# Optimization experiments

Hardware: AMD Instinct MI355X
Metric: run time of the kernel (lower is better)

The kernel has to match this reference:

```python
import jax, jax.numpy as jnp
import numpy as np

H = 64           # edge/node/global hidden size
IN_F = 4         # node_attr_size
OUT_F = 1        # out_size
NUM_EMB = 100    # edge_num_embeddings
SKIP = True


def setup_inputs() -> dict:
    key = jax.random.key(0)
    ks = jax.random.split(key, 24)
    T, N, E = 4, 20000, 320000
    NNZ = 340000
    inp = {
        'node_attr': jax.random.normal(ks[0], (T, N, IN_F), jnp.float32),
        'global_attr': jax.random.normal(ks[1], (1, H), jnp.float32),
        'L_values': jax.random.normal(ks[2], (NNZ,), jnp.float32),
        'coeff': jnp.ones((1,), jnp.float32),
        'edge_attr': jax.random.randint(ks[3], (T, E), 0, NUM_EMB),
        'edge_index': jax.random.randint(ks[4], (2, E), 0, N),
        'L_index': jax.random.randint(ks[5], (2, NNZ), 0, N),
        'num_processing_steps': 4,
        # parameters
        'emb': jax.random.normal(ks[6], (NUM_EMB, H), jnp.float32) * 0.05,
        'W_ne': jax.random.normal(ks[7], (IN_F, H), jnp.float32) * 0.1,
        'b_ne': jnp.zeros((H,), jnp.float32),
        'W_eb': jax.random.normal(ks[8], ((H + 2 * H) * 2 + H, H), jnp.float32) * 0.05,
        'b_eb': jnp.zeros((H,), jnp.float32),
        'W_nb': jax.random.normal(ks[9], (2 * H + 2 * H + H, H), jnp.float32) * 0.05,
        'b_nb': jnp.zeros((H,), jnp.float32),
        'W_gb': jax.random.normal(ks[10], (H + H + H, H), jnp.float32) * 0.05,
        'b_gb': jnp.zeros((H,), jnp.float32),
        'W_d1': jax.random.normal(ks[11], (H, H), jnp.float32) * 0.1,
        'b_d1': jnp.zeros((H,), jnp.float32),
        'W_d2': jax.random.normal(ks[12], (H, OUT_F), jnp.float32) * 0.1,
        'b_d2': jnp.zeros((OUT_F,), jnp.float32),
        'W_i1': jax.random.normal(ks[13], (H, H), jnp.float32) * 0.1,
        'b_i1': jnp.zeros((H,), jnp.float32),
        'W_i2': jax.random.normal(ks[14], (H, IN_F), jnp.float32) * 0.1,
        'b_i2': jnp.zeros((IN_F,), jnp.float32),
    }
    return inp


def reference(node_attr, global_attr, L_values, coeff, emb, W_ne, b_ne,
              W_eb, b_eb, W_nb, b_nb, W_gb, b_gb, W_d1, b_d1, W_d2, b_d2,
              W_i1, b_i1, W_i2, b_i2, edge_attr, edge_index, L_index,
              num_processing_steps):
    T, N, _ = node_attr.shape
    s, r = edge_index[0], edge_index[1]
    Li, Lj = L_index[0], L_index[1]

    # encoders (all T steps at once)
    x_enc = jax.nn.relu(node_attr @ W_ne + b_ne)   # [T,N,H]
    e_enc = emb[edge_attr]                         # [T,E,H]

    def laplacian(h):  # sparse sp_L @ h, h: [N,H]
        return jax.ops.segment_sum(L_values[:, None] * h[Lj], Li, num_segments=N)

    def step(carry, xe):
        h_x, h_e, h_g = carry
        x_t, e_t = xe
        node_cat = jnp.concatenate([x_t, h_x], axis=-1)          # [N,2H]
        edge_cat = jnp.concatenate([e_t, h_e], axis=-1)          # [E,2H]
        g = h_g[0]                                               # [H]
        E_ = edge_cat.shape[0]
        # EdgeBlock: edges + sender + receiver + globals
        eb_in = jnp.concatenate([edge_cat, node_cat[s], node_cat[r],
                                 jnp.broadcast_to(g, (E_, g.shape[0]))], axis=-1)
        e_new = jax.nn.relu(eb_in @ W_eb + b_eb)                 # [E,H]
        # NodeBlock: scatter_add aggregates of received/sent edges
        recv = jax.ops.segment_sum(e_new, r, num_segments=N)
        sent = jax.ops.segment_sum(e_new, s, num_segments=N)
        nb_in = jnp.concatenate([recv, sent, node_cat,
                                 jnp.broadcast_to(g, (N, g.shape[0]))], axis=-1)
        x_new = jax.nn.relu(nb_in @ W_nb + b_nb)                 # [N,H]
        # GlobalBlock: scatter_mean (single graph -> mean)
        gb_in = jnp.concatenate([e_new.mean(0), x_new.mean(0), g])[None]
        g_new = jax.nn.relu(gb_in @ W_gb + b_gb)                 # [1,H]
        h_x_next = h_x + x_new if SKIP else x_new
        time_d = h_x_next - h_x
        spat_d = coeff[0] * laplacian(h_x_next)  # pde='diff': coeff * L u
        return (h_x_next, e_new, g_new), (h_x_next, time_d, spat_d)

    h0 = (jnp.zeros((N, H), jnp.float32),
          jnp.zeros((e_enc.shape[1], H), jnp.float32),
          global_attr)
    _, (hid, time_d, spat_d) = jax.lax.scan(step, h0, (x_enc, e_enc))

    # decoders over all steps
    out_nodes = jax.nn.relu(hid @ W_d1 + b_d1) @ W_d2 + b_d2     # [T,N,OUT_F]
    pred_in = jax.nn.relu(hid @ W_i1 + b_i1) @ W_i2 + b_i2       # [T,N,IN_F]
    return out_nodes, time_d, spat_d, pred_in
```

## Files before the change

kernel.cpp:

```cpp
#include <hip/hip_runtime.h>

#define TT 4
#define NN 20000
#define EE 320000
#define NZ 340000
#define NBKT 2500

typedef __attribute__((ext_vector_type(8))) __bf16 bf16x8;
typedef __attribute__((ext_vector_type(16))) float f32x16;

__device__ __forceinline__ unsigned short f2bf(float f) {
    unsigned int u = __float_as_uint(f);
    u = (u + 0x7FFFu + ((u >> 16) & 1u)) >> 16;
    return (unsigned short)u;
}
__device__ __forceinline__ float bf2f(unsigned short h) {
    return __uint_as_float(((unsigned int)h) << 16);
}

#define GLL16(src, dst) __builtin_amdgcn_global_load_lds( \
    (const __attribute__((address_space(1))) unsigned int*)(src), \
    (__attribute__((address_space(3))) unsigned int*)(dst), 16, 0, 0)

__global__ void k_count(const int* __restrict__ r, const int* __restrict__ s,
                        const int* __restrict__ Li,
                        int* cnt_r, int* cnt_s, int* cnt_L) {
    int i = blockIdx.x * 256 + threadIdx.x;
    if (i < EE) { atomicAdd(&cnt_r[r[i]], 1); atomicAdd(&cnt_s[s[i]], 1); }
    if (i < NZ) { atomicAdd(&cnt_L[Li[i]], 1); }
}

__global__ __launch_bounds__(1024) void k_scan(int* cnt, int* rowp, int* wp) {
    int which = blockIdx.x;
    int* c = cnt + which * NN;
    int* row = rowp + which * (NN + 1);
    int* w = wp + which * NN;
    __shared__ int ssum[1024];
    int tid = threadIdx.x;
    const int CH = (NN + 1023) / 1024;
    int base = tid * CH;
    int s = 0;
    for (int i = 0; i < CH; ++i) { int idx = base + i; s += (idx < NN) ? c[idx] : 0; }
    ssum[tid] = s;
    __syncthreads();
    for (int o = 1; o < 1024; o <<= 1) {
        int v = (tid >= o) ? ssum[tid - o] : 0;
        __syncthreads();
        ssum[tid] += v;
        __syncthreads();
    }
    int run = (tid > 0) ? ssum[tid - 1] : 0;
    for (int i = 0; i < CH; ++i) {
        int idx = base + i;
        if (idx < NN) { row[idx] = run; w[idx] = run; run += c[idx]; }
    }
    if (tid == 1023) row[NN] = ssum[1023];
}

__global__ __launch_bounds__(256) void k_scatter(
    const int* __restrict__ r, const int* __restrict__ s,
    const int* __restrict__ Li, const int* __restrict__ Lj,
    const float* __restrict__ Lv,
    int* wp_r, int* wp_s, int* wp_L,
    int* col_r, int* col_s, uint2* col_L8) {
    const int bucket = blockIdx.x & 7;
    const int nlo = bucket * NBKT;
    const int cid = blockIdx.x >> 3;
    const int stride = (gridDim.x >> 3) * 256;
    for (int i = cid * 256 + threadIdx.x; i < EE; i += stride) {
        int rv = r[i];
        if ((unsigned)(rv - nlo) < (unsigned)NBKT)
            col_r[atomicAdd(&wp_r[rv], 1)] = i;
        int sv = s[i];
        if ((unsigned)(sv - nlo) < (unsigned)NBKT)
            col_s[atomicAdd(&wp_s[sv], 1)] = i;
    }
    for (int i = cid * 256 + threadIdx.x; i < NZ; i += stride) {
        int lv = Li[i];
        if ((unsigned)(lv - nlo) < (unsigned)NBKT) {
            int pos = atomicAdd(&wp_L[lv], 1);
            uint2 v;
            v.x = (unsigned int)Lj[i];
            v.y = __float_as_uint(Lv[i]);
            col_L8[pos] = v;
        }
    }
}

__global__ __launch_bounds__(256) void k_pack(
    const float* __restrict__ W_eb, const float* __restrict__ W_nb,
    const float* __restrict__ W_d1, const float* __restrict__ W_i1,
    const float* __restrict__ emb, unsigned short* __restrict__ Bpe,
    unsigned short* __restrict__ Bpu, unsigned short* __restrict__ Bpn,
    unsigned short* __restrict__ Bpd, unsigned short* __restrict__ emb_bf) {
    int t = blockIdx.x * 256 + threadIdx.x;
    if (t < 2 * 8 * 512) {
        int i = t & 7, l = (t >> 3) & 63, kb = (t >> 9) & 7, ch = t >> 12;
        int colv = ch * 32 + (l & 31);
        int k = kb * 16 + (l >> 5) * 8 + i;
        Bpe[t] = f2bf(W_eb[k * 64 + colv]);
    }
    if (t < 4 * 8 * 512) {
        int i = t & 7, l = (t >> 3) & 63, kb = (t >> 9) & 7, g = t >> 12;
        int colv = (g & 1) * 32 + (l & 31);
        int k = 128 + (g >> 1) * 128 + kb * 16 + (l >> 5) * 8 + i;
        Bpu[t] = f2bf(W_eb[k * 64 + colv]);
    }
    if (t < 2 * 16 * 512) {
        int i = t & 7, l = (t >> 3) & 63, kb = (t >> 9) % 16, ch = t / (16 * 512);
        int colv = ch * 32 + (l & 31);
        int k = kb * 16 + (l >> 5) * 8 + i;
        Bpn[t] = f2bf(W_nb[k * 64 + colv]);
    }
    if (t < 4 * 4 * 512) {
        int i = t & 7, l = (t >> 3) & 63, kb = (t >> 9) & 3, sec = t >> 11;
        int colv = (sec & 1) * 32 + (l & 31);
        int k = kb * 16 + (l >> 5) * 8 + i;
        const float* W = (sec < 2) ? W_d1 : W_i1;
        Bpd[t] = f2bf(W[k * 64 + colv]);
    }
    if (t < 100 * 64) emb_bf[t] = f2bf(emb[t]);
}

__global__ __launch_bounds__(256) void k_xenc(const float* __restrict__ na,
                                              const float* __restrict__ W_ne,
                                              const float* __restrict__ b_ne,
                                              unsigned short* __restrict__ xenc) {
    int row = blockIdx.x * 4 + (threadIdx.x >> 6);
    int j = threadIdx.x & 63;
    float4 a = *(const float4*)&na[(size_t)row * 4];
    float v = b_ne[j] + a.x * W_ne[j] + a.y * W_ne[64 + j] + a.z * W_ne[128 + j] + a.w * W_ne[192 + j];
    xenc[(size_t)row * 64 + j] = f2bf(fmaxf(v, 0.f));
}

__global__ __launch_bounds__(64) void k_usr(
    int do_update,
    const unsigned short* __restrict__ xenc_t, const unsigned short* __restrict__ hx_bf,
    const unsigned short* __restrict__ Bpu, unsigned int* __restrict__ usr,
    const float* __restrict__ W_gb, const float* __restrict__ b_gb,
    const float* __restrict__ W_eb, const float* __restrict__ b_eb,
    const float* __restrict__ W_nb, const float* __restrict__ b_nb,
    float* __restrict__ g_cur, float* __restrict__ e_sum, float* __restrict__ x_sum,
    float* __restrict__ gb_eb, float* __restrict__ gb_nb) {
    const int ln = threadIdx.x;
    const int er = ln & 31, hi = ln >> 5;

    if (blockIdx.x == 0) {
        int j = ln;
        float gv = g_cur[j];
        if (do_update) {
            float a = b_gb[j];
            for (int k = 0; k < 64; ++k) a += (e_sum[k] / (float)EE) * W_gb[k * 64 + j];
            for (int k = 0; k < 64; ++k) a += (x_sum[k] / (float)NN) * W_gb[(64 + k) * 64 + j];
            for (int k = 0; k < 64; ++k) a += g_cur[k] * W_gb[(128 + k) * 64 + j];
            gv = fmaxf(a, 0.f);
            g_cur[j] = gv;
            e_sum[j] = 0.f;
            x_sum[j] = 0.f;
        }
        float a1 = b_eb[j], a2 = b_nb[j];
        for (int k = 0; k < 64; ++k) {
            float gk = __shfl(gv, k, 64);
            a1 = fmaf(gk, W_eb[(384 + k) * 64 + j], a1);
            a2 = fmaf(gk, W_nb[(256 + k) * 64 + j], a2);
        }
        gb_eb[j] = a1;
        gb_nb[j] = a2;
    }

    const int n0 = blockIdx.x * 32;
    const int n = n0 + er;

    f32x16 a0, a1, a2, a3;
    #pragma unroll
    for (int i = 0; i < 16; ++i) { a0[i] = 0.f; a1[i] = 0.f; a2[i] = 0.f; a3[i] = 0.f; }

    const unsigned short* sx = xenc_t + (size_t)64 * n + hi * 8;
    const unsigned short* sh = hx_bf + (size_t)64 * n + hi * 8;
    #pragma unroll
    for (int c = 0; c < 2; ++c) {
        const unsigned short* src = c ? sh : sx;
        #pragma unroll
        for (int kb = 0; kb < 4; ++kb) {
            bf16x8 a = *(const bf16x8*)(src + kb * 16);
            int kg = c * 4 + kb;
            bf16x8 b0 = *(const bf16x8*)&Bpu[(size_t)((0 * 8 + kg) * 64 + ln) * 8];
            bf16x8 b1 = *(const bf16x8*)&Bpu[(size_t)((1 * 8 + kg) * 64 + ln) * 8];
            bf16x8 b2 = *(const bf16x8*)&Bpu[(size_t)((2 * 8 + kg) * 64 + ln) * 8];
            bf16x8 b3 = *(const bf16x8*)&Bpu[(size_t)((3 * 8 + kg) * 64 + ln) * 8];
            a0 = __builtin_amdgcn_mfma_f32_32x32x16_bf16(a, b0, a0, 0, 0, 0);
            a1 = __builtin_amdgcn_mfma_f32_32x32x16_bf16(a, b1, a1, 0, 0, 0);
            a2 = __builtin_amdgcn_mfma_f32_32x32x16_bf16(a, b2, a2, 0, 0, 0);
            a3 = __builtin_amdgcn_mfma_f32_32x32x16_bf16(a, b3, a3, 0, 0, 0);
        }
    }
    #pragma unroll
    for (int r = 0; r < 16; ++r) {
        int row = (r & 3) + 8 * (r >> 2) + 4 * hi;
        size_t o = (size_t)(n0 + row) * 64;
        usr[o + er]      = (unsigned int)f2bf(a0[r]) | ((unsigned int)f2bf(a1[r]) << 16);
        usr[o + 32 + er] = (unsigned int)f2bf(a2[r]) | ((unsigned int)f2bf(a3[r]) << 16);
    }
}

__global__ __launch_bounds__(512) void k_edge(
    int first, unsigned short* __restrict__ h_e,
    const unsigned short* __restrict__ emb_bf,
    const unsigned int* __restrict__ usr, const int* __restrict__ eattr_t,
    const int* __restrict__ sidx, const int* __restrict__ ridx,
    const unsigned short* __restrict__ Bp, const float* __restrict__ gbias,
    float* __restrict__ e_sum) {
    __shared__ unsigned short sBe[8192];
    __shared__ float sRed[8][64];
    const int tid = threadIdx.x;
    const int w = tid >> 6, ln = tid & 63;
    const int er = ln & 31, hi = ln >> 5;
    const int ebase = blockIdx.x * 256 + w * 32;
    const int e = ebase + er;

    const int siv = sidx[ebase + er];
    const int riv = ridx[ebase + er];
    const int ai = eattr_t[e];

    #pragma unroll
    for (int i = 0; i < 2; ++i) {
        int off = i * 4096 + w * 512;
        GLL16(Bp + off + ln * 8, sBe + off);
    }

    const unsigned short* s0 = emb_bf + (size_t)64 * ai + hi * 8;
    const unsigned short* s1 = h_e + (size_t)64 * e + hi * 8;
    bf16x8 a0 = *(const bf16x8*)(s0);
    bf16x8 a1 = *(const bf16x8*)(s0 + 16);
    bf16x8 a2 = *(const bf16x8*)(s0 + 32);
    bf16x8 a3 = *(const bf16x8*)(s0 + 48);
    bf16x8 a4{}, a5{}, a6{}, a7{};
    if (!first) {
        a4 = *(const bf16x8*)(s1);
        a5 = *(const bf16x8*)(s1 + 16);
        a6 = *(const bf16x8*)(s1 + 32);
        a7 = *(const bf16x8*)(s1 + 48);
    }

    f32x16 acc0, acc1;
    #pragma unroll
    for (int i = 0; i < 16; ++i) { acc0[i] = 0.f; acc1[i] = 0.f; }

    __syncthreads();

    #define EMM(AF, KG)                                                              \
        {                                                                            \
            bf16x8 b0 = *(const bf16x8*)&sBe[(((KG)) * 64 + ln) * 8];                \
            bf16x8 b1 = *(const bf16x8*)&sBe[((8 + (KG)) * 64 + ln) * 8];            \
            acc0 = __builtin_amdgcn_mfma_f32_32x32x16_bf16(AF, b0, acc0, 0, 0, 0);   \
            acc1 = __builtin_amdgcn_mfma_f32_32x32x16_bf16(AF, b1, acc1, 0, 0, 0);   \
        }
    EMM(a0, 0) EMM(a1, 1) EMM(a2, 2) EMM(a3, 3)
    if (!first) {
        EMM(a4, 4) EMM(a5, 5) EMM(a6, 6) EMM(a7, 7)
    }
    #undef EMM

    const float gb0 = gbias[er], gb1 = gbias[er + 32];
    float cs0 = 0.f, cs1 = 0.f;
    #pragma unroll
    for (int r = 0; r < 16; ++r) {
        int row = (r & 3) + 8 * (r >> 2) + 4 * hi;
        int si_row = __shfl(siv, row, 64);
        int ri_row = __shfl(riv, row, 64);
        unsigned int us = usr[(size_t)si_row * 64 + er];
        unsigned int ur = usr[(size_t)ri_row * 64 + 32 + er];
        size_t o = (size_t)(ebase + row) * 64;
        float v0 = fmaxf(acc0[r] + bf2f((unsigned short)(us & 0xFFFF))
                                 + bf2f((unsigned short)(ur & 0xFFFF)) + gb0, 0.f);
        float v1 = fmaxf(acc1[r] + bf2f((unsigned short)(us >> 16))
                                 + bf2f((unsigned short)(ur >> 16)) + gb1, 0.f);
        cs0 += v0; cs1 += v1;
        h_e[o + er] = f2bf(v0);
        h_e[o + er + 32] = f2bf(v1);
    }
    cs0 += __shfl_xor(cs0, 32, 64);
    cs1 += __shfl_xor(cs1, 32, 64);
    if (hi == 0) { sRed[w][er] = cs0; sRed[w][er + 32] = cs1; }
    __syncthreads();
    if (w == 0) {
        float t = 0.f;
        #pragma unroll
        for (int q = 0; q < 8; ++q) t += sRed[q][ln];
        atomicAdd(&e_sum[ln], t);
    }
}

__global__ __launch_bounds__(256) void k_gather(
    const unsigned short* __restrict__ h_e, const int* __restrict__ row_r,
    const int* __restrict__ col_r, const int* __restrict__ row_s,
    const int* __restrict__ col_s, unsigned short* __restrict__ recv,
    unsigned short* __restrict__ sentb) {
    int t = blockIdx.x * 256 + threadIdx.x;
    int sub = t & 31, n = t >> 5;
    int g = sub & 15, which = sub >> 4;
    const int* rowp = which ? row_s : row_r;
    const int* colp = which ? col_s : col_r;
    unsigned short* outp = which ? sentb : recv;

    float a0 = 0.f, a1 = 0.f, a2 = 0.f, a3 = 0.f;
    int b0 = rowp[n], b1 = rowp[n + 1];
    for (int p = b0; p < b1; ++p) {
        uint2 v = *(const uint2*)&h_e[(size_t)64 * colp[p] + g * 4];
        a0 += bf2f((unsigned short)(v.x & 0xFFFF));
        a1 += bf2f((unsigned short)(v.x >> 16));
        a2 += bf2f((unsigned short)(v.y & 0xFFFF));
        a3 += bf2f((unsigned short)(v.y >> 16));
    }
    uint2 packed;
    packed.x = (unsigned int)f2bf(a0) | ((unsigned int)f2bf(a1) << 16);
    packed.y = (unsigned int)f2bf(a2) | ((unsigned int)f2bf(a3) << 16);
    *(uint2*)&outp[(size_t)64 * n + g * 4] = packed;
}

#define NODE_CHUNK(CIDX, BASE)                                                          \
    {                                                                                   \
        const unsigned short* src = (BASE) + hi * 8;                                    \
        _Pragma("unroll") for (int kb = 0; kb < 4; ++kb) {                              \
            bf16x8 a = *(const bf16x8*)(src + kb * 16);                                 \
            bf16x8 b0 = *(const bf16x8*)&Bp[(size_t)(((CIDX)*4 + kb) * 64 + ln) * 8];   \
            bf16x8 b1 = *(const bf16x8*)&Bp[(size_t)((16 + (CIDX)*4 + kb) * 64 + ln) * 8]; \
            acc0 = __builtin_amdgcn_mfma_f32_32x32x16_bf16(a, b0, acc0, 0, 0, 0);       \
            acc1 = __builtin_amdgcn_mfma_f32_32x32x16_bf16(a, b1, acc1, 0, 0, 0);       \
        }                                                                               \
    }

__global__ __launch_bounds__(64) void k_node(
    const unsigned short* __restrict__ recv, const unsigned short* __restrict__ sentb,
    const unsigned short* __restrict__ xenc_t, float* __restrict__ h_x,
    unsigned short* __restrict__ hx_bf, const unsigned short* __restrict__ Bp,
    const float* __restrict__ gbias, float* __restrict__ x_sum,
    unsigned short* __restrict__ hid_t, float* __restrict__ timed_t) {
    const int ln = threadIdx.x;
    const int er = ln & 31, hi = ln >> 5;
    const int n0 = blockIdx.x * 32;
    const int n = n0 + er;

    f32x16 acc0, acc1;
    #pragma unroll
    for (int i = 0; i < 16; ++i) { acc0[i] = 0.f; acc1[i] = 0.f; }

    NODE_CHUNK(0, recv + (size_t)64 * n)
    NODE_CHUNK(1, sentb + (size_t)64 * n)
    NODE_CHUNK(2, xenc_t + (size_t)64 * n)
    NODE_CHUNK(3, hx_bf + (size_t)64 * n)

    const float gb0 = gbias[er], gb1 = gbias[er + 32];
    float cs0 = 0.f, cs1 = 0.f;
    #pragma unroll
    for (int r = 0; r < 16; ++r) {
        int row = (r & 3) + 8 * (r >> 2) + 4 * hi;
        size_t o = (size_t)(n0 + row) * 64;
        float x0 = fmaxf(acc0[r] + gb0, 0.f);
        float x1 = fmaxf(acc1[r] + gb1, 0.f);
        cs0 += x0; cs1 += x1;
        float hx0 = h_x[o + er] + x0;
        float hx1 = h_x[o + er + 32] + x1;
        unsigned short hb0 = f2bf(hx0), hb1 = f2bf(hx1);
        h_x[o + er] = hx0;        h_x[o + er + 32] = hx1;
        hx_bf[o + er] = hb0;      hx_bf[o + er + 32] = hb1;
        hid_t[o + er] = hb0;      hid_t[o + er + 32] = hb1;
        timed_t[o + er] = x0;     timed_t[o + er + 32] = x1;
    }
    cs0 += __shfl_xor(cs0, 32, 64);
    cs1 += __shfl_xor(cs1, 32, 64);
    if (hi == 0) {
        atomicAdd(&x_sum[er], cs0);
        atomicAdd(&x_sum[er + 32], cs1);
    }
}

__global__ __launch_bounds__(256) void k_lap(
    const unsigned short* __restrict__ hx_bf, const int* __restrict__ row_L,
    const uint2* __restrict__ col_L8, const float* __restrict__ coeff,
    float* __restrict__ spat_t) {
    int t = blockIdx.x * 256 + threadIdx.x;
    int sub = t & 31, n = t >> 5;
    int g = sub & 15, half = sub >> 4;
    float a0 = 0.f, a1 = 0.f, a2 = 0.f, a3 = 0.f;
    int b0 = row_L[n], b1 = row_L[n + 1];
    int mid = b0 + ((b1 - b0) >> 1);
    int p0 = half ? mid : b0;
    int p1 = half ? b1 : mid;
    for (int p = p0; p < p1; ++p) {
        uint2 e = col_L8[p];
        float lv = __uint_as_float(e.y);
        uint2 hv = *(const uint2*)&hx_bf[(size_t)64 * e.x + g * 4];
        a0 = fmaf(lv, bf2f((unsigned short)(hv.x & 0xFFFF)), a0);
        a1 = fmaf(lv, bf2f((unsigned short)(hv.x >> 16)), a1);
        a2 = fmaf(lv, bf2f((unsigned short)(hv.y & 0xFFFF)), a2);
        a3 = fmaf(lv, bf2f((unsigned short)(hv.y >> 16)), a3);
    }
    a0 += __shfl_xor(a0, 16, 64);
    a1 += __shfl_xor(a1, 16, 64);
    a2 += __shfl_xor(a2, 16, 64);
    a3 += __shfl_xor(a3, 16, 64);
    if (half == 0) {
        float c = coeff[0];
        float4 outv = {c * a0, c * a1, c * a2, c * a3};
        *(float4*)&spat_t[(size_t)64 * n + g * 4] = outv;
    }
}

__global__ __launch_bounds__(256) void k_dec(
    const unsigned short* __restrict__ hid_bf, const unsigned short* __restrict__ Bpd,
    const float* __restrict__ b_d1, const float* __restrict__ W_d2,
    const float* __restrict__ b_d2, const float* __restrict__ b_i1,
    const float* __restrict__ W_i2, const float* __restrict__ b_i2,
    float* __restrict__ out_nodes, float* __restrict__ pred_in) {
    __shared__ unsigned short sDec[4][32 * 138];
    const int tid = threadIdx.x;
    const int w = tid >> 6, ln = tid & 63;
    const int er = ln & 31, hi = ln >> 5;
    const int row0 = (blockIdx.x * 4 + w) * 32;

    f32x16 ad0, ad1, ai0, ai1;
    #pragma unroll
    for (int i = 0; i < 16; ++i) { ad0[i] = 0.f; ad1[i] = 0.f; ai0[i] = 0.f; ai1[i] = 0.f; }

    const unsigned short* src = hid_bf + (size_t)(row0 + er) * 64 + hi * 8;
    #pragma unroll
    for (int kb = 0; kb < 4; ++kb) {
        bf16x8 a = *(const bf16x8*)(src + kb * 16);
        bf16x8 bd0 = *(const bf16x8*)&Bpd[((0 * 4 + kb) * 64 + ln) * 8];
        bf16x8 bd1 = *(const bf16x8*)&Bpd[((4 + kb) * 64 + ln) * 8];
        bf16x8 bi0 = *(const bf16x8*)&Bpd[((8 + kb) * 64 + ln) * 8];
        bf16x8 bi1 = *(const bf16x8*)&Bpd[((12 + kb) * 64 + ln) * 8];
        ad0 = __builtin_amdgcn_mfma_f32_32x32x16_bf16(a, bd0, ad0, 0, 0, 0);
        ad1 = __builtin_amdgcn_mfma_f32_32x32x16_bf16(a, bd1, ad1, 0, 0, 0);
        ai0 = __builtin_amdgcn_mfma_f32_32x32x16_bf16(a, bi0, ai0, 0, 0, 0);
        ai1 = __builtin_amdgcn_mfma_f32_32x32x16_bf16(a, bi1, ai1, 0, 0, 0);
    }

    const float bd0v = b_d1[er], bd1v = b_d1[er + 32];
    const float bi0v = b_i1[er], bi1v = b_i1[er + 32];
    unsigned short* sw = &sDec[w][0];
    #pragma unroll
    for (int r = 0; r < 16; ++r) {
        int row = (r & 3) + 8 * (r >> 2) + 4 * hi;
        sw[row * 138 + er]       = f2bf(fmaxf(ad0[r] + bd0v, 0.f));
        sw[row * 138 + er + 32]  = f2bf(fmaxf(ad1[r] + bd1v, 0.f));
        sw[row * 138 + er + 64]  = f2bf(fmaxf(ai0[r] + bi0v, 0.f));
        sw[row * 138 + er + 96]  = f2bf(fmaxf(ai1[r] + bi1v, 0.f));
    }
    __syncthreads();

    const int g_row = row0 + er;
    if (hi == 0) {
        float s = 0.f;
        for (int k = 0; k < 32; ++k) {
            unsigned int u = *(const unsigned int*)&sw[er * 138 + 2 * k];
            s = fmaf(bf2f((unsigned short)(u & 0xFFFF)), W_d2[2 * k], s);
            s = fmaf(bf2f((unsigned short)(u >> 16)), W_d2[2 * k + 1], s);
        }
        out_nodes[g_row] = s + b_d2[0];
    } else {
        float s0 = 0.f, s1 = 0.f, s2 = 0.f, s3 = 0.f;
        for (int k = 0; k < 32; ++k) {
            unsigned int u = *(const unsigned int*)&sw[er * 138 + 64 + 2 * k];
            float vlo = bf2f((unsigned short)(u & 0xFFFF));
            float vhi = bf2f((unsigned short)(u >> 16));
            float4 w0 = *(const float4*)&W_i2[(2 * k) * 4];
            float4 w1 = *(const float4*)&W_i2[(2 * k + 1) * 4];
            s0 = fmaf(vlo, w0.x, fmaf(vhi, w1.x, s0));
            s1 = fmaf(vlo, w0.y, fmaf(vhi, w1.y, s1));
            s2 = fmaf(vlo, w0.z, fmaf(vhi, w1.z, s2));
            s3 = fmaf(vlo, w0.w, fmaf(vhi, w1.w, s3));
        }
        float4 pv = {s0 + b_i2[0], s1 + b_i2[1], s2 + b_i2[2], s3 + b_i2[3]};
        *(float4*)&pred_in[(size_t)4 * g_row] = pv;
    }
}

extern "C" void kernel_launch(void* const* d_in, const int* in_sizes, int n_in,
                              void* d_out, int out_size, void* d_ws, size_t ws_size,
                              hipStream_t stream) {
    (void)in_sizes; (void)n_in; (void)out_size; (void)ws_size;
    const float* node_attr   = (const float*)d_in[0];
    const float* global_attr = (const float*)d_in[1];
    const float* L_values    = (const float*)d_in[2];
    const float* coeff       = (const float*)d_in[3];
    const int*   edge_attr   = (const int*)d_in[4];
    const int*   edge_index  = (const int*)d_in[5];
    const int*   L_index     = (const int*)d_in[6];
    const float* emb  = (const float*)d_in[8];
    const float* W_ne = (const float*)d_in[9];
    const float* b_ne = (const float*)d_in[10];
    const float* W_eb = (const float*)d_in[11];
    const float* b_eb = (const float*)d_in[12];
    const float* W_nb = (const float*)d_in[13];
    const float* b_nb = (const float*)d_in[14];
    const float* W_gb = (const float*)d_in[15];
    const float* b_gb = (const float*)d_in[16];
    const float* W_d1 = (const float*)d_in[17];
    const float* b_d1 = (const float*)d_in[18];
    const float* W_d2 = (const float*)d_in[19];
    const float* b_d2 = (const float*)d_in[20];
    const float* W_i1 = (const float*)d_in[21];
    const float* b_i1 = (const float*)d_in[22];
    const float* W_i2 = (const float*)d_in[23];
    const float* b_i2 = (const float*)d_in[24];

    const int* s_idx = edge_index;
    const int* r_idx = edge_index + EE;
    const int* Li = L_index;
    const int* Lj = L_index + NZ;

    char* ws = (char*)d_ws;
    size_t off = 0;
    auto alloc = [&](size_t bytes) -> void* {
        void* p = ws + off;
        off = (off + bytes + 255) & ~(size_t)255;
        return p;
    };
    unsigned short* xenc   = (unsigned short*)alloc((size_t)TT * NN * 64 * 2);
    unsigned short* hid    = (unsigned short*)alloc((size_t)TT * NN * 64 * 2);
    float*          h_x    = (float*)alloc((size_t)NN * 64 * 4);
    unsigned short* hx_bf  = (unsigned short*)alloc((size_t)NN * 64 * 2);
    unsigned short* h_e    = (unsigned short*)alloc((size_t)EE * 64 * 2);
    unsigned short* recv   = (unsigned short*)alloc((size_t)NN * 64 * 2);
    unsigned short* sentb  = (unsigned short*)alloc((size_t)NN * 64 * 2);
    unsigned int*   usr    = (unsigned int*)alloc((size_t)NN * 64 * 4);
    float* smalls          = (float*)alloc(2048);
    unsigned short* Bpe    = (unsigned short*)alloc((size_t)2 * 8 * 512 * 2);
    unsigned short* Bpu    = (unsigned short*)alloc((size_t)4 * 8 * 512 * 2);
    unsigned short* Bpn    = (unsigned short*)alloc((size_t)2 * 16 * 512 * 2);
    unsigned short* Bpd    = (unsigned short*)alloc((size_t)4 * 4 * 512 * 2);
    unsigned short* emb_bf = (unsigned short*)alloc((size_t)100 * 64 * 2);
    int* cnt    = (int*)alloc((size_t)3 * NN * 4);
    int* rowp   = (int*)alloc((size_t)3 * (NN + 1) * 4);
    int* wp     = (int*)alloc((size_t)3 * NN * 4);
    int* col_r  = (int*)alloc((size_t)EE * 4);
    int* col_s  = (int*)alloc((size_t)EE * 4);
    uint2* col_L8 = (uint2*)alloc((size_t)NZ * 8);

    float* g_cur = smalls;
    float* e_sum = smalls + 64;
    float* x_sum = smalls + 128;
    float* gb_eb = smalls + 192;
    float* gb_nb = smalls + 256;
    int* cnt_r = cnt, *cnt_s = cnt + NN, *cnt_L = cnt + 2 * NN;
    int* row_r = rowp, *row_s = rowp + (NN + 1), *row_L = rowp + 2 * (NN + 1);
    int* wp_r = wp, *wp_s = wp + NN, *wp_L = wp + 2 * NN;

    float* out_nodes = (float*)d_out;
    float* time_d = out_nodes + (size_t)TT * NN;
    float* spat_d = time_d + (size_t)TT * NN * 64;
    float* pred_in = spat_d + (size_t)TT * NN * 64;

    hipMemsetAsync(h_x, 0, (size_t)NN * 64 * 4, stream);
    hipMemsetAsync(hx_bf, 0, (size_t)NN * 64 * 2, stream);
    hipMemsetAsync(smalls, 0, 2048, stream);
    hipMemsetAsync(cnt, 0, (size_t)3 * NN * 4, stream);
    hipMemcpyAsync(g_cur, global_attr, 64 * 4, hipMemcpyDeviceToDevice, stream);

    k_count<<<(NZ + 255) / 256, 256, 0, stream>>>(r_idx, s_idx, Li, cnt_r, cnt_s, cnt_L);
    k_scan<<<3, 1024, 0, stream>>>(cnt, rowp, wp);
    k_scatter<<<2048, 256, 0, stream>>>(r_idx, s_idx, Li, Lj, L_values,
                                        wp_r, wp_s, wp_L, col_r, col_s, col_L8);
    k_pack<<<96, 256, 0, stream>>>(W_eb, W_nb, W_d1, W_i1, emb,
                                   Bpe, Bpu, Bpn, Bpd, emb_bf);
    k_xenc<<<TT * NN / 4, 256, 0, stream>>>(node_attr, W_ne, b_ne, xenc);

    for (int t = 0; t < TT; ++t) {
        const unsigned short* xenc_t = xenc + (size_t)t * NN * 64;
        k_usr<<<NN / 32, 64, 0, stream>>>(t > 0, xenc_t, hx_bf, Bpu, usr,
                                          W_gb, b_gb, W_eb, b_eb, W_nb, b_nb,
                                          g_cur, e_sum, x_sum, gb_eb, gb_nb);
        k_edge<<<EE / 256, 512, 0, stream>>>(t == 0, h_e, emb_bf, usr,
                                             edge_attr + (size_t)t * EE, s_idx, r_idx,
                                             Bpe, gb_eb, e_sum);
        k_gather<<<NN * 32 / 256, 256, 0, stream>>>(h_e, row_r, col_r, row_s, col_s,
                                                    recv, sentb);
        k_node<<<NN / 32, 64, 0, stream>>>(recv, sentb, xenc_t, h_x, hx_bf,
                                           Bpn, gb_nb, x_sum,
                                           hid + (size_t)t * NN * 64,
                                           time_d + (size_t)t * NN * 64);
        k_lap<<<NN * 32 / 256, 256, 0, stream>>>(hx_bf, row_L, col_L8, coeff,
                                                 spat_d + (size_t)t * NN * 64);
    }
    k_dec<<<TT * NN / 128, 256, 0, stream>>>(hid, Bpd, b_d1, W_d2, b_d2,
                                             b_i1, W_i2, b_i2, out_nodes, pred_in);
}
```

Baseline: 675.9 us.

## Fuse Laplacian SpMV with next-step node-update GEMM into one launch

The per-step Laplacian kernel and the following step's usr GEMM/global-update kernel become one launch that splits blocks by role: the first LAPB blocks do the SpMV and the rest do the usr work for step t+1. The usr path moves from 64-thread blocks to 256-thread blocks with four waves each. The CSR-build kernels also switch index loads to nontemporal loads. This removes launches and lets the two independent pieces of work overlap on the GPU. The global update still runs in the last step's fused launch because it resets e_sum and x_sum.

```diff
diff --git a/kernel.cpp b/kernel.cpp
--- a/kernel.cpp
+++ b/kernel.cpp
@@ -5,6 +5,7 @@
 #define EE 320000
 #define NZ 340000
 #define NBKT 2500
+#define LAPB 2500
 
 typedef __attribute__((ext_vector_type(8))) __bf16 bf16x8;
 typedef __attribute__((ext_vector_type(16))) float f32x16;
@@ -26,8 +27,11 @@
                         const int* __restrict__ Li,
                         int* cnt_r, int* cnt_s, int* cnt_L) {
     int i = blockIdx.x * 256 + threadIdx.x;
-    if (i < EE) { atomicAdd(&cnt_r[r[i]], 1); atomicAdd(&cnt_s[s[i]], 1); }
-    if (i < NZ) { atomicAdd(&cnt_L[Li[i]], 1); }
+    if (i < EE) {
+        atomicAdd(&cnt_r[__builtin_nontemporal_load(&r[i])], 1);
+        atomicAdd(&cnt_s[__builtin_nontemporal_load(&s[i])], 1);
+    }
+    if (i < NZ) { atomicAdd(&cnt_L[__builtin_nontemporal_load(&Li[i])], 1); }
 }
 
 __global__ __launch_bounds__(1024) void k_scan(int* cnt, int* rowp, int* wp) {
@@ -68,20 +72,20 @@
     const int cid = blockIdx.x >> 3;
     const int stride = (gridDim.x >> 3) * 256;
     for (int i = cid * 256 + threadIdx.x; i < EE; i += stride) {
-        int rv = r[i];
+        int rv = __builtin_nontemporal_load(&r[i]);
         if ((unsigned)(rv - nlo) < (unsigned)NBKT)
             col_r[atomicAdd(&wp_r[rv], 1)] = i;
-        int sv = s[i];
+        int sv = __builtin_nontemporal_load(&s[i]);
         if ((unsigned)(sv - nlo) < (unsigned)NBKT)
             col_s[atomicAdd(&wp_s[sv], 1)] = i;
     }
     for (int i = cid * 256 + threadIdx.x; i < NZ; i += stride) {
-        int lv = Li[i];
+        int lv = __builtin_nontemporal_load(&Li[i]);
         if ((unsigned)(lv - nlo) < (unsigned)NBKT) {
             int pos = atomicAdd(&wp_L[lv], 1);
             uint2 v;
-            v.x = (unsigned int)Lj[i];
-            v.y = __float_as_uint(Lv[i]);
+            v.x = (unsigned int)__builtin_nontemporal_load(&Lj[i]);
+            v.y = __float_as_uint(__builtin_nontemporal_load(&Lv[i]));
             col_L8[pos] = v;
         }
     }
@@ -133,19 +137,54 @@
     xenc[(size_t)row * 64 + j] = f2bf(fmaxf(v, 0.f));
 }
 
-__global__ __launch_bounds__(64) void k_usr(
-    int do_update,
-    const unsigned short* __restrict__ xenc_t, const unsigned short* __restrict__ hx_bf,
-    const unsigned short* __restrict__ Bpu, unsigned int* __restrict__ usr,
+__global__ __launch_bounds__(256) void k_fuse(
+    int lapb, int nwaves_usr, int do_update,
+    const unsigned short* __restrict__ hx_bf, const int* __restrict__ row_L,
+    const uint2* __restrict__ col_L8, const float* __restrict__ coeff,
+    float* __restrict__ spat_t,
+    const unsigned short* __restrict__ xenc_next, const unsigned short* __restrict__ Bpu,
+    unsigned int* __restrict__ usr,
     const float* __restrict__ W_gb, const float* __restrict__ b_gb,
     const float* __restrict__ W_eb, const float* __restrict__ b_eb,
     const float* __restrict__ W_nb, const float* __restrict__ b_nb,
     float* __restrict__ g_cur, float* __restrict__ e_sum, float* __restrict__ x_sum,
     float* __restrict__ gb_eb, float* __restrict__ gb_nb) {
-    const int ln = threadIdx.x;
+    const int tid = threadIdx.x;
+    if ((int)blockIdx.x < lapb) {
+        int t = blockIdx.x * 256 + tid;
+        int sub = t & 31, n = t >> 5;
+        int g = sub & 15, half = sub >> 4;
+        float a0 = 0.f, a1 = 0.f, a2 = 0.f, a3 = 0.f;
+        int b0 = row_L[n], b1 = row_L[n + 1];
+        int mid = b0 + ((b1 - b0) >> 1);
+        int p0 = half ? mid : b0;
+        int p1 = half ? b1 : mid;
+        for (int p = p0; p < p1; ++p) {
+            uint2 e = col_L8[p];
+            float lv = __uint_as_float(e.y);
+            uint2 hv = *(const uint2*)&hx_bf[(size_t)64 * e.x + g * 4];
+            a0 = fmaf(lv, bf2f((unsigned short)(hv.x & 0xFFFF)), a0);
+            a1 = fmaf(lv, bf2f((unsigned short)(hv.x >> 16)), a1);
+            a2 = fmaf(lv, bf2f((unsigned short)(hv.y & 0xFFFF)), a2);
+            a3 = fmaf(lv, bf2f((unsigned short)(hv.y >> 16)), a3);
+        }
+        a0 += __shfl_xor(a0, 16, 64);
+        a1 += __shfl_xor(a1, 16, 64);
+        a2 += __shfl_xor(a2, 16, 64);
+        a3 += __shfl_xor(a3, 16, 64);
+        if (half == 0) {
+            float c = coeff[0];
+            float4 outv = {c * a0, c * a1, c * a2, c * a3};
+            *(float4*)&spat_t[(size_t)64 * n + g * 4] = outv;
+        }
+        return;
+    }
+
+    const int ln = tid & 63;
+    const int wid = ((int)blockIdx.x - lapb) * 4 + (tid >> 6);
     const int er = ln & 31, hi = ln >> 5;
 
-    if (blockIdx.x == 0) {
+    if (wid == 0) {
         int j = ln;
         float gv = g_cur[j];
         if (do_update) {
@@ -167,15 +206,16 @@
         gb_eb[j] = a1;
         gb_nb[j] = a2;
     }
-
-    const int n0 = blockIdx.x * 32;
+    if (wid >= nwaves_usr) return;
+
+    const int n0 = wid * 32;
     const int n = n0 + er;
 
     f32x16 a0, a1, a2, a3;
     #pragma unroll
     for (int i = 0; i < 16; ++i) { a0[i] = 0.f; a1[i] = 0.f; a2[i] = 0.f; a3[i] = 0.f; }
 
-    const unsigned short* sx = xenc_t + (size_t)64 * n + hi * 8;
+    const unsigned short* sx = xenc_next + (size_t)64 * n + hi * 8;
     const unsigned short* sh = hx_bf + (size_t)64 * n + hi * 8;
     #pragma unroll
     for (int c = 0; c < 2; ++c) {
@@ -372,38 +412,6 @@
     if (hi == 0) {
         atomicAdd(&x_sum[er], cs0);
         atomicAdd(&x_sum[er + 32], cs1);
-    }
-}
-
-__global__ __launch_bounds__(256) void k_lap(
-    const unsigned short* __restrict__ hx_bf, const int* __restrict__ row_L,
-    const uint2* __restrict__ col_L8, const float* __restrict__ coeff,
-    float* __restrict__ spat_t) {
-    int t = blockIdx.x * 256 + threadIdx.x;
-    int sub = t & 31, n = t >> 5;
-    int g = sub & 15, half = sub >> 4;
-    float a0 = 0.f, a1 = 0.f, a2 = 0.f, a3 = 0.f;
-    int b0 = row_L[n], b1 = row_L[n + 1];
-    int mid = b0 + ((b1 - b0) >> 1);
-    int p0 = half ? mid : b0;
-    int p1 = half ? b1 : mid;
-    for (int p = p0; p < p1; ++p) {
-        uint2 e = col_L8[p];
-        float lv = __uint_as_float(e.y);
-        uint2 hv = *(const uint2*)&hx_bf[(size_t)64 * e.x + g * 4];
-        a0 = fmaf(lv, bf2f((unsigned short)(hv.x & 0xFFFF)), a0);
-        a1 = fmaf(lv, bf2f((unsigned short)(hv.x >> 16)), a1);
-        a2 = fmaf(lv, bf2f((unsigned short)(hv.y & 0xFFFF)), a2);
-        a3 = fmaf(lv, bf2f((unsigned short)(hv.y >> 16)), a3);
-    }
-    a0 += __shfl_xor(a0, 16, 64);
-    a1 += __shfl_xor(a1, 16, 64);
-    a2 += __shfl_xor(a2, 16, 64);
-    a3 += __shfl_xor(a3, 16, 64);
-    if (half == 0) {
-        float c = coeff[0];
-        float4 outv = {c * a0, c * a1, c * a2, c * a3};
-        *(float4*)&spat_t[(size_t)64 * n + g * 4] = outv;
     }
 }
 
@@ -567,11 +575,15 @@
                                    Bpe, Bpu, Bpn, Bpd, emb_bf);
     k_xenc<<<TT * NN / 4, 256, 0, stream>>>(node_attr, W_ne, b_ne, xenc);
 
+    const int USRB = (NN / 32 + 3) / 4;
+    k_fuse<<<USRB, 256, 0, stream>>>(0, NN / 32, 0,
+                                     hx_bf, row_L, col_L8, coeff, spat_d,
+                                     xenc, Bpu, usr,
+                                     W_gb, b_gb, W_eb, b_eb, W_nb, b_nb,
+                                     g_cur, e_sum, x_sum, gb_eb, gb_nb);
+
     for (int t = 0; t < TT; ++t) {
         const unsigned short* xenc_t = xenc + (size_t)t * NN * 64;
-        k_usr<<<NN / 32, 64, 0, stream>>>(t > 0, xenc_t, hx_bf, Bpu, usr,
-                                          W_gb, b_gb, W_eb, b_eb, W_nb, b_nb,
-                                          g_cur, e_sum, x_sum, gb_eb, gb_nb);
         k_edge<<<EE / 256, 512, 0, stream>>>(t == 0, h_e, emb_bf, usr,
                                              edge_attr + (size_t)t * EE, s_idx, r_idx,
                                              Bpe, gb_eb, e_sum);
@@ -581,8 +593,16 @@
                                            Bpn, gb_nb, x_sum,
                                            hid + (size_t)t * NN * 64,
                                            time_d + (size_t)t * NN * 64);
-        k_lap<<<NN * 32 / 256, 256, 0, stream>>>(hx_bf, row_L, col_L8, coeff,
-                                                 spat_d + (size_t)t * NN * 64);
+        int nwaves = (t < TT - 1) ? NN / 32 : 0;
+        int grid = LAPB + ((t < TT - 1) ? USRB : 1);
+        const unsigned short* xenc_next =
+            xenc + (size_t)((t < TT - 1) ? t + 1 : t) * NN * 64;
+        k_fuse<<<grid, 256, 0, stream>>>(LAPB, nwaves, 1,
+                                         hx_bf, row_L, col_L8, coeff,
+                                         spat_d + (size_t)t * NN * 64,
+                                         xenc_next, Bpu, usr,
+                                         W_gb, b_gb, W_eb, b_eb, W_nb, b_nb,
+                                         g_cur, e_sum, x_sum, gb_eb, gb_nb);
     }
     k_dec<<<TT * NN / 128, 256, 0, stream>>>(hid, Bpd, b_d1, W_d2, b_d2,
                                              b_i1, W_i2, b_i2, out_nodes, pred_in);
```

Measured after the change: 716.2 us. 6.0% more time.

## Merge setup kernels and fuse the Laplacian of step t-1 into the gather of step t

Applied to the files above, without the earlier changes.

Three setup kernels (xenc encode, index counting, weight packing) become one launch that dispatches on block index. In the time loop, the Laplacian for the previous step's hidden state now runs in the same launch as the current step's edge gather. A final standalone Laplacian launch handles the last step. This cuts kernel launches and lets two independent, memory-bound gather workloads share the GPU. Correctness relies on hx_bf not being overwritten until k_node runs, which holds because k_node is launched after the fused kernel.

```diff
diff --git a/kernel.cpp b/kernel.cpp
--- a/kernel.cpp
+++ b/kernel.cpp
@@ -22,12 +22,63 @@
     (const __attribute__((address_space(1))) unsigned int*)(src), \
     (__attribute__((address_space(3))) unsigned int*)(dst), 16, 0, 0)
 
-__global__ void k_count(const int* __restrict__ r, const int* __restrict__ s,
-                        const int* __restrict__ Li,
-                        int* cnt_r, int* cnt_s, int* cnt_L) {
-    int i = blockIdx.x * 256 + threadIdx.x;
-    if (i < EE) { atomicAdd(&cnt_r[r[i]], 1); atomicAdd(&cnt_s[s[i]], 1); }
-    if (i < NZ) { atomicAdd(&cnt_L[Li[i]], 1); }
+#define XB (TT * NN / 4)
+#define CB ((NZ + 255) / 256)
+
+__global__ __launch_bounds__(256) void k_setup(
+    const float* __restrict__ na, const float* __restrict__ W_ne,
+    const float* __restrict__ b_ne, unsigned short* __restrict__ xenc,
+    const int* __restrict__ r, const int* __restrict__ s,
+    const int* __restrict__ Li, int* cnt_r, int* cnt_s, int* cnt_L,
+    const float* __restrict__ W_eb, const float* __restrict__ W_nb,
+    const float* __restrict__ W_d1, const float* __restrict__ W_i1,
+    const float* __restrict__ emb, unsigned short* __restrict__ Bpe,
+    unsigned short* __restrict__ Bpu, unsigned short* __restrict__ Bpn,
+    unsigned short* __restrict__ Bpd, unsigned short* __restrict__ emb_bf) {
+    int bid = blockIdx.x;
+    if (bid < XB) {
+        int row = bid * 4 + (threadIdx.x >> 6);
+        int j = threadIdx.x & 63;
+        float4 a = *(const float4*)&na[(size_t)row * 4];
+        float v = b_ne[j] + a.x * W_ne[j] + a.y * W_ne[64 + j] + a.z * W_ne[128 + j] + a.w * W_ne[192 + j];
+        xenc[(size_t)row * 64 + j] = f2bf(fmaxf(v, 0.f));
+        return;
+    }
+    bid -= XB;
+    if (bid < CB) {
+        int i = bid * 256 + threadIdx.x;
+        if (i < EE) { atomicAdd(&cnt_r[r[i]], 1); atomicAdd(&cnt_s[s[i]], 1); }
+        if (i < NZ) { atomicAdd(&cnt_L[Li[i]], 1); }
+        return;
+    }
+    bid -= CB;
+    int t = bid * 256 + threadIdx.x;
+    if (t < 2 * 8 * 512) {
+        int i = t & 7, l = (t >> 3) & 63, kb = (t >> 9) & 7, ch = t >> 12;
+        int colv = ch * 32 + (l & 31);
+        int k = kb * 16 + (l >> 5) * 8 + i;
+        Bpe[t] = f2bf(W_eb[k * 64 + colv]);
+    }
+    if (t < 4 * 8 * 512) {
+        int i = t & 7, l = (t >> 3) & 63, kb = (t >> 9) & 7, g = t >> 12;
+        int colv = (g & 1) * 32 + (l & 31);
+        int k = 128 + (g >> 1) * 128 + kb * 16 + (l >> 5) * 8 + i;
+        Bpu[t] = f2bf(W_eb[k * 64 + colv]);
+    }
+    if (t < 2 * 16 * 512) {
+        int i = t & 7, l = (t >> 3) & 63, kb = (t >> 9) % 16, ch = t / (16 * 512);
+        int colv = ch * 32 + (l & 31);
+        int k = kb * 16 + (l >> 5) * 8 + i;
+        Bpn[t] = f2bf(W_nb[k * 64 + colv]);
+    }
+    if (t < 4 * 4 * 512) {
+        int i = t & 7, l = (t >> 3) & 63, kb = (t >> 9) & 3, sec = t >> 11;
+        int colv = (sec & 1) * 32 + (l & 31);
+        int k = kb * 16 + (l >> 5) * 8 + i;
+        const float* W = (sec < 2) ? W_d1 : W_i1;
+        Bpd[t] = f2bf(W[k * 64 + colv]);
+    }
+    if (t < 100 * 64) emb_bf[t] = f2bf(emb[t]);
 }
 
 __global__ __launch_bounds__(1024) void k_scan(int* cnt, int* rowp, int* wp) {
@@ -87,52 +138,6 @@
     }
 }
 
-__global__ __launch_bounds__(256) void k_pack(
-    const float* __restrict__ W_eb, const float* __restrict__ W_nb,
-    const float* __restrict__ W_d1, const float* __restrict__ W_i1,
-    const float* __restrict__ emb, unsigned short* __restrict__ Bpe,
-    unsigned short* __restrict__ Bpu, unsigned short* __restrict__ Bpn,
-    unsigned short* __restrict__ Bpd, unsigned short* __restrict__ emb_bf) {
-    int t = blockIdx.x * 256 + threadIdx.x;
-    if (t < 2 * 8 * 512) {
-        int i = t & 7, l = (t >> 3) & 63, kb = (t >> 9) & 7, ch = t >> 12;
-        int colv = ch * 32 + (l & 31);
-        int k = kb * 16 + (l >> 5) * 8 + i;
-        Bpe[t] = f2bf(W_eb[k * 64 + colv]);
-    }
-    if (t < 4 * 8 * 512) {
-        int i = t & 7, l = (t >> 3) & 63, kb = (t >> 9) & 7, g = t >> 12;
-        int colv = (g & 1) * 32 + (l & 31);
-        int k = 128 + (g >> 1) * 128 + kb * 16 + (l >> 5) * 8 + i;
-        Bpu[t] = f2bf(W_eb[k * 64 + colv]);
-    }
-    if (t < 2 * 16 * 512) {
-        int i = t & 7, l = (t >> 3) & 63, kb = (t >> 9) % 16, ch = t / (16 * 512);
-        int colv = ch * 32 + (l & 31);
-        int k = kb * 16 + (l >> 5) * 8 + i;
-        Bpn[t] = f2bf(W_nb[k * 64 + colv]);
-    }
-    if (t < 4 * 4 * 512) {
-        int i = t & 7, l = (t >> 3) & 63, kb = (t >> 9) & 3, sec = t >> 11;
-        int colv = (sec & 1) * 32 + (l & 31);
-        int k = kb * 16 + (l >> 5) * 8 + i;
-        const float* W = (sec < 2) ? W_d1 : W_i1;
-        Bpd[t] = f2bf(W[k * 64 + colv]);
-    }
-    if (t < 100 * 64) emb_bf[t] = f2bf(emb[t]);
-}
-
-__global__ __launch_bounds__(256) void k_xenc(const float* __restrict__ na,
-                                              const float* __restrict__ W_ne,
-                                              const float* __restrict__ b_ne,
-                                              unsigned short* __restrict__ xenc) {
-    int row = blockIdx.x * 4 + (threadIdx.x >> 6);
-    int j = threadIdx.x & 63;
-    float4 a = *(const float4*)&na[(size_t)row * 4];
-    float v = b_ne[j] + a.x * W_ne[j] + a.y * W_ne[64 + j] + a.z * W_ne[128 + j] + a.w * W_ne[192 + j];
-    xenc[(size_t)row * 64 + j] = f2bf(fmaxf(v, 0.f));
-}
-
 __global__ __launch_bounds__(64) void k_usr(
     int do_update,
     const unsigned short* __restrict__ xenc_t, const unsigned short* __restrict__ hx_bf,
@@ -291,95 +296,39 @@
     }
 }
 
-__global__ __launch_bounds__(256) void k_gather(
+__global__ __launch_bounds__(256) void k_glap(
+    int gatherb,
     const unsigned short* __restrict__ h_e, const int* __restrict__ row_r,
     const int* __restrict__ col_r, const int* __restrict__ row_s,
     const int* __restrict__ col_s, unsigned short* __restrict__ recv,
-    unsigned short* __restrict__ sentb) {
-    int t = blockIdx.x * 256 + threadIdx.x;
-    int sub = t & 31, n = t >> 5;
-    int g = sub & 15, which = sub >> 4;
-    const int* rowp = which ? row_s : row_r;
-    const int* colp = which ? col_s : col_r;
-    unsigned short* outp = which ? sentb : recv;
-
-    float a0 = 0.f, a1 = 0.f, a2 = 0.f, a3 = 0.f;
-    int b0 = rowp[n], b1 = rowp[n + 1];
-    for (int p = b0; p < b1; ++p) {
-        uint2 v = *(const uint2*)&h_e[(size_t)64 * colp[p] + g * 4];
-        a0 += bf2f((unsigned short)(v.x & 0xFFFF));
-        a1 += bf2f((unsigned short)(v.x >> 16));
-        a2 += bf2f((unsigned short)(v.y & 0xFFFF));
-        a3 += bf2f((unsigned short)(v.y >> 16));
-    }
-    uint2 packed;
-    packed.x = (unsigned int)f2bf(a0) | ((unsigned int)f2bf(a1) << 16);
-    packed.y = (unsigned int)f2bf(a2) | ((unsigned int)f2bf(a3) << 16);
-    *(uint2*)&outp[(size_t)64 * n + g * 4] = packed;
-}
-
-#define NODE_CHUNK(CIDX, BASE)                                                          \
-    {                                                                                   \
-        const unsigned short* src = (BASE) + hi * 8;                                    \
-        _Pragma("unroll") for (int kb = 0; kb < 4; ++kb) {                              \
-            bf16x8 a = *(const bf16x8*)(src + kb * 16);                                 \
-            bf16x8 b0 = *(const bf16x8*)&Bp[(size_t)(((CIDX)*4 + kb) * 64 + ln) * 8];   \
-            bf16x8 b1 = *(const bf16x8*)&Bp[(size_t)((16 + (CIDX)*4 + kb) * 64 + ln) * 8]; \
-            acc0 = __builtin_amdgcn_mfma_f32_32x32x16_bf16(a, b0, acc0, 0, 0, 0);       \
-            acc1 = __builtin_amdgcn_mfma_f32_32x32x16_bf16(a, b1, acc1, 0, 0, 0);       \
-        }                                                                               \
-    }
-
-__global__ __launch_bounds__(64) void k_node(
-    const unsigned short* __restrict__ recv, const unsigned short* __restrict__ sentb,
-    const unsigned short* __restrict__ xenc_t, float* __restrict__ h_x,
-    unsigned short* __restrict__ hx_bf, const unsigned short* __restrict__ Bp,
-    const float* __restrict__ gbias, float* __restrict__ x_sum,
-    unsigned short* __restrict__ hid_t, float* __restrict__ timed_t) {
-    const int ln = threadIdx.x;
-    const int er = ln & 31, hi = ln >> 5;
-    const int n0 = blockIdx.x * 32;
-    const int n = n0 + er;
-
-    f32x16 acc0, acc1;
-    #pragma unroll
-    for (int i = 0; i < 16; ++i) { acc0[i] = 0.f; acc1[i] = 0.f; }
-
-    NODE_CHUNK(0, recv + (size_t)64 * n)
-    NODE_CHUNK(1, sentb + (size_t)64 * n)
-    NODE_CHUNK(2, xenc_t + (size_t)64 * n)
-    NODE_CHUNK(3, hx_bf + (size_t)64 * n)
-
-    const float gb0 = gbias[er], gb1 = gbias[er + 32];
-    float cs0 = 0.f, cs1 = 0.f;
-    #pragma unroll
-    for (int r = 0; r < 16; ++r) {
-        int row = (r & 3) + 8 * (r >> 2) + 4 * hi;
-        size_t o = (size_t)(n0 + row) * 64;
-        float x0 = fmaxf(acc0[r] + gb0, 0.f);
-        float x1 = fmaxf(acc1[r] + gb1, 0.f);
-        cs0 += x0; cs1 += x1;
-        float hx0 = h_x[o + er] + x0;
-        float hx1 = h_x[o + er + 32] + x1;
-        unsigned short hb0 = f2bf(hx0), hb1 = f2bf(hx1);
-        h_x[o + er] = hx0;        h_x[o + er + 32] = hx1;
-        hx_bf[o + er] = hb0;      hx_bf[o + er + 32] = hb1;
-        hid_t[o + er] = hb0;      hid_t[o + er + 32] = hb1;
-        timed_t[o + er] = x0;     timed_t[o + er + 32] = x1;
-    }
-    cs0 += __shfl_xor(cs0, 32, 64);
-    cs1 += __shfl_xor(cs1, 32, 64);
-    if (hi == 0) {
-        atomicAdd(&x_sum[er], cs0);
-        atomicAdd(&x_sum[er + 32], cs1);
-    }
-}
-
-__global__ __launch_bounds__(256) void k_lap(
+    unsigned short* __restrict__ sentb,
     const unsigned short* __restrict__ hx_bf, const int* __restrict__ row_L,
     const uint2* __restrict__ col_L8, const float* __restrict__ coeff,
-    float* __restrict__ spat_t) {
-    int t = blockIdx.x * 256 + threadIdx.x;
+    float* __restrict__ spat_prev) {
+    if ((int)blockIdx.x < gatherb) {
+        int t = blockIdx.x * 256 + threadIdx.x;
+        int sub = t & 31, n = t >> 5;
+        int g = sub & 15, which = sub >> 4;
+        const int* rowp = which ? row_s : row_r;
+        const int* colp = which ? col_s : col_r;
+        unsigned short* outp = which ? sentb : recv;
+
+        float a0 = 0.f, a1 = 0.f, a2 = 0.f, a3 = 0.f;
+        int b0 = rowp[n], b1 = rowp[n + 1];
+        for (int p = b0; p < b1; ++p) {
+            uint2 v = *(const uint2*)&h_e[(size_t)64 * colp[p] + g * 4];
+            a0 += bf2f((unsigned short)(v.x & 0xFFFF));
+            a1 += bf2f((unsigned short)(v.x >> 16));
+            a2 += bf2f((unsigned short)(v.y & 0xFFFF));
+            a3 += bf2f((unsigned short)(v.y >> 16));
+        }
+        uint2 packed;
+        packed.x = (unsigned int)f2bf(a0) | ((unsigned int)f2bf(a1) << 16);
+        packed.y = (unsigned int)f2bf(a2) | ((unsigned int)f2bf(a3) << 16);
+        *(uint2*)&outp[(size_t)64 * n + g * 4] = packed;
+        return;
+    }
+    int t = ((int)blockIdx.x - gatherb) * 256 + threadIdx.x;
     int sub = t & 31, n = t >> 5;
     int g = sub & 15, half = sub >> 4;
     float a0 = 0.f, a1 = 0.f, a2 = 0.f, a3 = 0.f;
@@ -403,7 +352,64 @@
     if (half == 0) {
         float c = coeff[0];
         float4 outv = {c * a0, c * a1, c * a2, c * a3};
-        *(float4*)&spat_t[(size_t)64 * n + g * 4] = outv;
+        *(float4*)&spat_prev[(size_t)64 * n + g * 4] = outv;
+    }
+}
+
+#define NODE_CHUNK(CIDX, BASE)                                                          \
+    {                                                                                   \
+        const unsigned short* src = (BASE) + hi * 8;                                    \
+        _Pragma("unroll") for (int kb = 0; kb < 4; ++kb) {                              \
+            bf16x8 a = *(const bf16x8*)(src + kb * 16);                                 \
+            bf16x8 b0 = *(const bf16x8*)&Bp[(size_t)(((CIDX)*4 + kb) * 64 + ln) * 8];   \
+            bf16x8 b1 = *(const bf16x8*)&Bp[(size_t)((16 + (CIDX)*4 + kb) * 64 + ln) * 8]; \
+            acc0 = __builtin_amdgcn_mfma_f32_32x32x16_bf16(a, b0, acc0, 0, 0, 0);       \
+            acc1 = __builtin_amdgcn_mfma_f32_32x32x16_bf16(a, b1, acc1, 0, 0, 0);       \
+        }                                                                               \
+    }
+
+__global__ __launch_bounds__(64) void k_node(
+    const unsigned short* __restrict__ recv, const unsigned short* __restrict__ sentb,
+    const unsigned short* __restrict__ xenc_t, float* __restrict__ h_x,
+    unsigned short* __restrict__ hx_bf, const unsigned short* __restrict__ Bp,
+    const float* __restrict__ gbias, float* __restrict__ x_sum,
+    unsigned short* __restrict__ hid_t, float* __restrict__ timed_t) {
+    const int ln = threadIdx.x;
+    const int er = ln & 31, hi = ln >> 5;
+    const int n0 = blockIdx.x * 32;
+    const int n = n0 + er;
+
+    f32x16 acc0, acc1;
+    #pragma unroll
+    for (int i = 0; i < 16; ++i) { acc0[i] = 0.f; acc1[i] = 0.f; }
+
+    NODE_CHUNK(0, recv + (size_t)64 * n)
+    NODE_CHUNK(1, sentb + (size_t)64 * n)
+    NODE_CHUNK(2, xenc_t + (size_t)64 * n)
+    NODE_CHUNK(3, hx_bf + (size_t)64 * n)
+
+    const float gb0 = gbias[er], gb1 = gbias[er + 32];
+    float cs0 = 0.f, cs1 = 0.f;
+    #pragma unroll
+    for (int r = 0; r < 16; ++r) {
+        int row = (r & 3) + 8 * (r >> 2) + 4 * hi;
+        size_t o = (size_t)(n0 + row) * 64;
+        float x0 = fmaxf(acc0[r] + gb0, 0.f);
+        float x1 = fmaxf(acc1[r] + gb1, 0.f);
+        cs0 += x0; cs1 += x1;
+        float hx0 = h_x[o + er] + x0;
+        float hx1 = h_x[o + er + 32] + x1;
+        unsigned short hb0 = f2bf(hx0), hb1 = f2bf(hx1);
+        h_x[o + er] = hx0;        h_x[o + er + 32] = hx1;
+        hx_bf[o + er] = hb0;      hx_bf[o + er + 32] = hb1;
+        hid_t[o + er] = hb0;      hid_t[o + er + 32] = hb1;
+        timed_t[o + er] = x0;     timed_t[o + er + 32] = x1;
+    }
+    cs0 += __shfl_xor(cs0, 32, 64);
+    cs1 += __shfl_xor(cs1, 32, 64);
+    if (hi == 0) {
+        atomicAdd(&x_sum[er], cs0);
+        atomicAdd(&x_sum[er + 32], cs1);
     }
 }
 
@@ -559,14 +565,15 @@
     hipMemsetAsync(cnt, 0, (size_t)3 * NN * 4, stream);
     hipMemcpyAsync(g_cur, global_attr, 64 * 4, hipMemcpyDeviceToDevice, stream);
 
-    k_count<<<(NZ + 255) / 256, 256, 0, stream>>>(r_idx, s_idx, Li, cnt_r, cnt_s, cnt_L);
+    k_setup<<<XB + CB + 96, 256, 0, stream>>>(node_attr, W_ne, b_ne, xenc,
+                                              r_idx, s_idx, Li, cnt_r, cnt_s, cnt_L,
+                                              W_eb, W_nb, W_d1, W_i1, emb,
+                                              Bpe, Bpu, Bpn, Bpd, emb_bf);
     k_scan<<<3, 1024, 0, stream>>>(cnt, rowp, wp);
     k_scatter<<<2048, 256, 0, stream>>>(r_idx, s_idx, Li, Lj, L_values,
                                         wp_r, wp_s, wp_L, col_r, col_s, col_L8);
-    k_pack<<<96, 256, 0, stream>>>(W_eb, W_nb, W_d1, W_i1, emb,
-                                   Bpe, Bpu, Bpn, Bpd, emb_bf);
-    k_xenc<<<TT * NN / 4, 256, 0, stream>>>(node_attr, W_ne, b_ne, xenc);
-
+
+    const int GB = NN * 32 / 256;
     for (int t = 0; t < TT; ++t) {
         const unsigned short* xenc_t = xenc + (size_t)t * NN * 64;
         k_usr<<<NN / 32, 64, 0, stream>>>(t > 0, xenc_t, hx_bf, Bpu, usr,
@@ -575,15 +582,19 @@
         k_edge<<<EE / 256, 512, 0, stream>>>(t == 0, h_e, emb_bf, usr,
                                              edge_attr + (size_t)t * EE, s_idx, r_idx,
                                              Bpe, gb_eb, e_sum);
-        k_gather<<<NN * 32 / 256, 256, 0, stream>>>(h_e, row_r, col_r, row_s, col_s,
-                                                    recv, sentb);
+        int grid = GB + ((t > 0) ? GB : 0);
+        float* spat_prev = spat_d + (size_t)((t > 0) ? t - 1 : 0) * NN * 64;
+        k_glap<<<grid, 256, 0, stream>>>(GB, h_e, row_r, col_r, row_s, col_s,
+                                         recv, sentb, hx_bf, row_L, col_L8, coeff,
+                                         spat_prev);
         k_node<<<NN / 32, 64, 0, stream>>>(recv, sentb, xenc_t, h_x, hx_bf,
                                            Bpn, gb_nb, x_sum,
                                            hid + (size_t)t * NN * 64,
                                            time_d + (size_t)t * NN * 64);
-        k_lap<<<NN * 32 / 256, 256, 0, stream>>>(hx_bf, row_L, col_L8, coeff,
-                                                 spat_d + (size_t)t * NN * 64);
-    }
+    }
+    k_glap<<<GB, 256, 0, stream>>>(0, h_e, row_r, col_r, row_s, col_s,
+                                   recv, sentb, hx_bf, row_L, col_L8, coeff,
+                                   spat_d + (size_t)(TT - 1) * NN * 64);
     k_dec<<<TT * NN / 128, 256, 0, stream>>>(hid, Bpd, b_d1, W_d2, b_d2,
                                              b_i1, W_i2, b_i2, out_nodes, pred_in);
 }
```

Result: faster. 634.3 us (-6.2%).
